# Kernel tuning notes

Measured on AMD Instinct MI355X. Metric: run time of the kernel, lower is better.

The kernel has to match this reference:

```python
import jax, jax.numpy as jnp
import numpy as np

NH = 16   # num_heads
HD = 128  # head_dim
HS = 2048 # hidden_size
LI, LT = 2048, 512
MLP = 4 * HS


def _ln(x, s, b):
    m = jnp.mean(x, axis=-1, keepdims=True)
    v = jnp.var(x, axis=-1, keepdims=True)
    return (x - m) * jax.lax.rsqrt(v + 1e-6) * s + b


def _rms(x, s):
    return x * jax.lax.rsqrt(jnp.mean(x * x, axis=-1, keepdims=True) + 1e-6) * s


def _mod6(vec, w, b):
    a = (jax.nn.silu(vec) @ w + b)[:, None, :]
    return jnp.split(a, 6, axis=-1)  # shift1,scale1,gate1,shift2,scale2,gate2


def _rope(x, pe):
    B, H, L, D = x.shape
    xr = x.reshape(B, H, L, D // 2, 1, 2)
    return (pe[..., 0] * xr[..., 0] + pe[..., 1] * xr[..., 1]).reshape(B, H, L, D)


def _attention(q, k, v, pe):
    q = _rope(q, pe)
    k = _rope(k, pe)
    scores = jnp.einsum('bhqd,bhkd->bhqk', q, k) * (q.shape[-1] ** -0.5)
    p = jax.nn.softmax(scores, axis=-1)
    o = jnp.einsum('bhqk,bhkd->bhqd', p, v)
    B, H, L, D = o.shape
    return o.transpose(0, 2, 1, 3).reshape(B, L, H * D)


def _prenorm_qkv(x, shift, scale, ln_s, ln_b, qkv_w, qkv_b, qn, kn):
    xm = (1.0 + scale) * _ln(x, ln_s, ln_b) + shift
    y = xm @ qkv_w + qkv_b
    B, L, _ = y.shape
    y = y.reshape(B, L, 3, NH, HD).transpose(2, 0, 3, 1, 4)  # K B H L D
    q, k, v = y[0], y[1], y[2]
    return _rms(q, qn), _rms(k, kn), v


def _forward(img, txt, vec, pe,
             img_mod_w, img_mod_b, img_norm1_s, img_norm1_b, img_qkv_w, img_qkv_b,
             img_qn_s, img_kn_s, img_proj_w, img_proj_b, img_norm2_s, img_norm2_b,
             img_mlp_w1, img_mlp_b1, img_mlp_w2, img_mlp_b2,
             txt_mod_w, txt_mod_b, txt_norm1_s, txt_norm1_b, txt_qkv_w, txt_qkv_b,
             txt_qn_s, txt_kn_s, txt_proj_w, txt_proj_b, txt_norm2_s, txt_norm2_b,
             txt_mlp_w1, txt_mlp_b1, txt_mlp_w2, txt_mlp_b2):
    i_sh1, i_sc1, i_g1, i_sh2, i_sc2, i_g2 = _mod6(vec, img_mod_w, img_mod_b)
    t_sh1, t_sc1, t_g1, t_sh2, t_sc2, t_g2 = _mod6(vec, txt_mod_w, txt_mod_b)

    iq, ik, iv = _prenorm_qkv(img, i_sh1, i_sc1, img_norm1_s, img_norm1_b,
                              img_qkv_w, img_qkv_b, img_qn_s, img_kn_s)
    tq, tk, tv = _prenorm_qkv(txt, t_sh1, t_sc1, txt_norm1_s, txt_norm1_b,
                              txt_qkv_w, txt_qkv_b, txt_qn_s, txt_kn_s)

    q = jnp.concatenate((tq, iq), axis=2)
    k = jnp.concatenate((tk, ik), axis=2)
    v = jnp.concatenate((tv, iv), axis=2)
    attn = _attention(q, k, v, pe)  # [B, LT+LI, HS]
    Lt = txt.shape[1]
    txt_attn, img_attn = attn[:, :Lt], attn[:, Lt:]

    img = img + i_g1 * (img_attn @ img_proj_w + img_proj_b)
    img_h = (1.0 + i_sc2) * _ln(img, img_norm2_s, img_norm2_b) + i_sh2
    img = img + i_g2 * (jax.nn.gelu(img_h @ img_mlp_w1 + img_mlp_b1) @ img_mlp_w2 + img_mlp_b2)

    txt = txt + t_g1 * (txt_attn @ txt_proj_w + txt_proj_b)
    txt_h = (1.0 + t_sc2) * _ln(txt, txt_norm2_s, txt_norm2_b) + t_sh2
    txt = txt + t_g2 * (jax.nn.gelu(txt_h @ txt_mlp_w1 + txt_mlp_b1) @ txt_mlp_w2 + txt_mlp_b2)
    return img, txt


def setup_inputs() -> dict:
    key = jax.random.key(0)
    ki = iter(jax.random.split(key, 48))
    def n(shape, s=0.02):
        return jax.random.normal(next(ki), shape, jnp.float32) * s
    d = {
        'img': jax.random.normal(next(ki), (1, LI, HS), jnp.float32),
        'txt': jax.random.normal(next(ki), (1, LT, HS), jnp.float32),
        'vec': jax.random.normal(next(ki), (1, HS), jnp.float32),
        'pe': jax.random.normal(next(ki), (1, 1, LT + LI, HD // 2, 2, 2), jnp.float32),
    }
    for p in ('img', 'txt'):
        d[p + '_mod_w'] = n((HS, 6 * HS)); d[p + '_mod_b'] = jnp.zeros((6 * HS,), jnp.float32)
        d[p + '_norm1_s'] = jnp.ones((HS,), jnp.float32); d[p + '_norm1_b'] = jnp.zeros((HS,), jnp.float32)
        d[p + '_qkv_w'] = n((HS, 3 * HS)); d[p + '_qkv_b'] = jnp.zeros((3 * HS,), jnp.float32)
        d[p + '_qn_s'] = jnp.ones((HD,), jnp.float32); d[p + '_kn_s'] = jnp.ones((HD,), jnp.float32)
        d[p + '_proj_w'] = n((HS, HS)); d[p + '_proj_b'] = jnp.zeros((HS,), jnp.float32)
        d[p + '_norm2_s'] = jnp.ones((HS,), jnp.float32); d[p + '_norm2_b'] = jnp.zeros((HS,), jnp.float32)
        d[p + '_mlp_w1'] = n((HS, MLP)); d[p + '_mlp_b1'] = jnp.zeros((MLP,), jnp.float32)
        d[p + '_mlp_w2'] = n((MLP, HS)); d[p + '_mlp_b2'] = jnp.zeros((HS,), jnp.float32)
    return d


def reference(img, txt, vec, pe,
              img_mod_w, img_mod_b, img_norm1_s, img_norm1_b, img_qkv_w, img_qkv_b,
              img_qn_s, img_kn_s, img_proj_w, img_proj_b, img_norm2_s, img_norm2_b,
              img_mlp_w1, img_mlp_b1, img_mlp_w2, img_mlp_b2,
              txt_mod_w, txt_mod_b, txt_norm1_s, txt_norm1_b, txt_qkv_w, txt_qkv_b,
              txt_qn_s, txt_kn_s, txt_proj_w, txt_proj_b, txt_norm2_s, txt_norm2_b,
              txt_mlp_w1, txt_mlp_b1, txt_mlp_w2, txt_mlp_b2):
    return _forward(img, txt, vec, pe,
                    img_mod_w, img_mod_b, img_norm1_s, img_norm1_b, img_qkv_w, img_qkv_b,
                    img_qn_s, img_kn_s, img_proj_w, img_proj_b, img_norm2_s, img_norm2_b,
                    img_mlp_w1, img_mlp_b1, img_mlp_w2, img_mlp_b2,
                    txt_mod_w, txt_mod_b, txt_norm1_s, txt_norm1_b, txt_qkv_w, txt_qkv_b,
                    txt_qn_s, txt_kn_s, txt_proj_w, txt_proj_b, txt_norm2_s, txt_norm2_b,
                    txt_mlp_w1, txt_mlp_b1, txt_mlp_w2, txt_mlp_b2)
```

## Files before the change

### kernel.cpp

```cpp
#include <hip/hip_runtime.h>
#include <hip/hip_bf16.h>
#include <math.h>

typedef __bf16 bf16;
typedef __bf16 bf16x2 __attribute__((ext_vector_type(2)));
typedef __bf16 bf16x8 __attribute__((ext_vector_type(8)));
typedef float f32x4 __attribute__((ext_vector_type(4)));

#define HS 2048
#define NH 16
#define HD 128
#define LT 512
#define LI 2048
#define LQ 2560
#define MLP_D 8192
#define SPLIT 4
#define KVS (LQ / SPLIT)
#define KVBLK 32
#define NTILES (KVS / KVBLK)

__device__ __forceinline__ f32x4 mfma16(bf16x8 a, bf16x8 b, f32x4 c) {
  return __builtin_amdgcn_mfma_f32_16x16x32_bf16(a, b, c, 0, 0, 0);
}

__device__ __forceinline__ void gl_lds16(const bf16* g, bf16* l) {
  __builtin_amdgcn_global_load_lds((const __attribute__((address_space(1))) void*)g,
                                   (__attribute__((address_space(3))) void*)l, 16, 0, 0);
}

__global__ void k_silu(const float* __restrict__ v, float* __restrict__ s) {
  int i = blockIdx.x * 256 + threadIdx.x;
  float x = v[i];
  s[i] = x / (1.f + expf(-x));
}

__global__ __launch_bounds__(256) void k_mod_partial(
    const float* __restrict__ s, const float* __restrict__ w_txt,
    const float* __restrict__ w_img, float* __restrict__ part) {
  int strm = blockIdx.x / 48;
  int n = (blockIdx.x % 48) * 256 + threadIdx.x;
  const float* w = strm ? w_img : w_txt;
  int k0 = blockIdx.y * 256;
  __shared__ float sl[256];
  sl[threadIdx.x] = s[k0 + threadIdx.x];
  __syncthreads();
  float acc = 0.f;
  for (int k = 0; k < 256; k++)
    acc += sl[k] * w[(size_t)(k0 + k) * 12288 + n];
  part[((size_t)blockIdx.y * 2 + strm) * 12288 + n] = acc;
}

__global__ __launch_bounds__(256) void k_mod_reduce(
    const float* __restrict__ part, const float* __restrict__ b_txt,
    const float* __restrict__ b_img, float* __restrict__ mod) {
  int strm = blockIdx.x / 48;
  int n = (blockIdx.x % 48) * 256 + threadIdx.x;
  float acc = strm ? b_img[n] : b_txt[n];
  for (int kc = 0; kc < 8; kc++)
    acc += part[((size_t)kc * 2 + strm) * 12288 + n];
  mod[(size_t)strm * 12288 + n] = acc;
}

__global__ __launch_bounds__(256) void k_transpose_cvt(
    const float* __restrict__ src, bf16* __restrict__ dst, int R, int C) {
  __shared__ float t[32][33];
  int tx = threadIdx.x & 31, ty = threadIdx.x >> 5;
  int c0 = blockIdx.x * 32, r0 = blockIdx.y * 32;
  for (int i = 0; i < 32; i += 8)
    t[ty + i][tx] = src[(size_t)(r0 + ty + i) * C + c0 + tx];
  __syncthreads();
  for (int i = 0; i < 32; i += 8)
    dst[(size_t)(c0 + ty + i) * R + r0 + tx] = (bf16)t[tx][ty + i];
}

__global__ __launch_bounds__(256) void k_ln_mod(
    const float* __restrict__ x0, const float* __restrict__ x1,
    const float* __restrict__ ls0, const float* __restrict__ lb0,
    const float* __restrict__ ls1, const float* __restrict__ lb1,
    const float* __restrict__ mod0, const float* __restrict__ mod1,
    int shidx, int scidx, bf16* __restrict__ out) {
  int r = blockIdx.x;
  int strm = r >= LT;
  const float* x = strm ? (x1 + (size_t)(r - LT) * HS) : (x0 + (size_t)r * HS);
  const float* ls = strm ? ls1 : ls0;
  const float* lb = strm ? lb1 : lb0;
  const float* md = strm ? mod1 : mod0;
  const float* sh = md + (size_t)shidx * HS;
  const float* sc = md + (size_t)scidx * HS;
  int t = threadIdx.x;
  float4 a = ((const float4*)x)[t * 2];
  float4 b = ((const float4*)x)[t * 2 + 1];
  float xv[8] = {a.x, a.y, a.z, a.w, b.x, b.y, b.z, b.w};
  float sum = 0.f, sq = 0.f;
#pragma unroll
  for (int j = 0; j < 8; j++) { sum += xv[j]; sq += xv[j] * xv[j]; }
#pragma unroll
  for (int m = 32; m; m >>= 1) { sum += __shfl_xor(sum, m); sq += __shfl_xor(sq, m); }
  __shared__ float red[8];
  int lane = t & 63, wid = t >> 6;
  if (!lane) { red[wid] = sum; red[wid + 4] = sq; }
  __syncthreads();
  float ts = red[0] + red[1] + red[2] + red[3];
  float tq = red[4] + red[5] + red[6] + red[7];
  float mean = ts * (1.f / HS);
  float var = tq * (1.f / HS) - mean * mean;
  float inv = rsqrtf(var + 1e-6f);
  int c0 = t * 8;
  bf16x8 ov;
#pragma unroll
  for (int j = 0; j < 8; j++) {
    int c = c0 + j;
    float v = ((xv[j] - mean) * inv * ls[c] + lb[c]) * (1.f + sc[c]) + sh[c];
    ov[j] = (bf16)v;
  }
  *(bf16x8*)(out + (size_t)r * HS + c0) = ov;
}

template <int MODE>
__global__ __launch_bounds__(256) void k_gemm(
    const bf16* __restrict__ A, int K, int N, int Ksz,
    const bf16* __restrict__ BT0, const bf16* __restrict__ BT1,
    const float* __restrict__ bias0, const float* __restrict__ bias1,
    void* __restrict__ out0, void* __restrict__ out1) {
  __shared__ bf16 As[128 * 32];
  __shared__ bf16 Bs[128 * 32];
  int tid = threadIdx.x;
  int bn = blockIdx.x, bm = blockIdx.y;
  int strm = (bm * 128) >= LT;
  int lm = bm * 128 - strm * LT;
  const bf16* BT = strm ? BT1 : BT0;
  int lane = tid & 63, wid = tid >> 6;
  int wr = wid >> 1, wc = wid & 1;
  int sr = tid >> 2, sc8 = (tid & 3) * 8;
  const bf16* Ag = A + (size_t)(bm * 128 + sr) * K + sc8;
  const bf16* Bg = BT + (size_t)(bn * 128 + sr) * K + sc8;
  bf16* As_dst = As + wid * 512;
  bf16* Bs_dst = Bs + wid * 512;
  int kbeg = MODE == 4 ? blockIdx.z * Ksz : 0;
  f32x4 acc[4][4] = {};
  for (int k0 = kbeg; k0 < kbeg + Ksz; k0 += 32) {
    __syncthreads();
    gl_lds16(Ag + k0, As_dst);
    gl_lds16(Ag + (size_t)64 * K + k0, As_dst + 2048);
    gl_lds16(Bg + k0, Bs_dst);
    gl_lds16(Bg + (size_t)64 * K + k0, Bs_dst + 2048);
    __syncthreads();
    bf16x8 af[4], bfr[4];
    int r16 = lane & 15, kc8 = (lane >> 4) * 8;
#pragma unroll
    for (int m = 0; m < 4; m++) af[m] = *(const bf16x8*)&As[(wr * 64 + m * 16 + r16) * 32 + kc8];
#pragma unroll
    for (int n = 0; n < 4; n++) bfr[n] = *(const bf16x8*)&Bs[(wc * 64 + n * 16 + r16) * 32 + kc8];
#pragma unroll
    for (int m = 0; m < 4; m++)
#pragma unroll
      for (int n = 0; n < 4; n++)
        acc[m][n] = mfma16(af[m], bfr[n], acc[m][n]);
  }
  int col = lane & 15, rb = (lane >> 4) * 4;
  const float* bias = strm ? bias1 : bias0;
  float* part = MODE == 4 ? (float*)out0 + (size_t)blockIdx.z * LQ * N : nullptr;
#pragma unroll
  for (int m = 0; m < 4; m++) {
#pragma unroll
    for (int n = 0; n < 4; n++) {
      int gn = bn * 128 + wc * 64 + n * 16 + col;
      float bv = MODE == 4 ? 0.f : bias[gn];
#pragma unroll
      for (int r = 0; r < 4; r++) {
        int lr = wr * 64 + m * 16 + rb + r;
        float v = acc[m][n][r] + bv;
        if (MODE == 0) {
          ((bf16*)(strm ? out1 : out0))[(size_t)(lm + lr) * N + gn] = (bf16)v;
        } else if (MODE == 2) {
          float g = 0.5f * v * (1.f + tanhf(0.7978845608028654f * (v + 0.044715f * v * v * v)));
          ((bf16*)(strm ? out1 : out0))[(size_t)(lm + lr) * N + gn] = (bf16)g;
        } else {
          part[(size_t)(bm * 128 + lr) * N + gn] = v;
        }
      }
    }
  }
}

template <int S>
__global__ __launch_bounds__(256) void k_skcomb(
    const float* __restrict__ part, int N,
    const float* __restrict__ bias0, const float* __restrict__ bias1,
    const float* __restrict__ gate0, const float* __restrict__ gate1,
    const float* __restrict__ res0, const float* __restrict__ res1,
    float* __restrict__ out0, float* __restrict__ out1) {
  int gid = blockIdx.x * 256 + threadIdx.x;
  int nv = N >> 2;
  int row = gid / nv, cv = gid - row * nv;
  int strm = row >= LT;
  int lrow = row - strm * LT;
  const float* bias = strm ? bias1 : bias0;
  const float* gate = strm ? gate1 : gate0;
  const float* res = strm ? res1 : res0;
  float* out = strm ? out1 : out0;
  int c = cv * 4;
  float4 acc = *(const float4*)(bias + c);
#pragma unroll
  for (int s = 0; s < S; s++) {
    float4 p = *(const float4*)(part + ((size_t)s * LQ + row) * N + c);
    acc.x += p.x; acc.y += p.y; acc.z += p.z; acc.w += p.w;
  }
  float4 g = *(const float4*)(gate + c);
  float4 r = *(const float4*)(res + (size_t)lrow * N + c);
  float4 o = {r.x + g.x * acc.x, r.y + g.y * acc.y, r.z + g.z * acc.z, r.w + g.w * acc.w};
  *(float4*)(out + (size_t)lrow * N + c) = o;
}

__global__ __launch_bounds__(256) void k_qkv_post(
    const bf16* __restrict__ y, const float* __restrict__ pe,
    const float* __restrict__ qn0, const float* __restrict__ kn0,
    const float* __restrict__ qn1, const float* __restrict__ kn1,
    bf16* __restrict__ qh, bf16* __restrict__ kh) {
  int wv = (int)((blockIdx.x * 256 + threadIdx.x) >> 6);
  int lane = threadIdx.x & 63;
  int head = wv / LQ, l = wv - head * LQ;
  const bf16* yr = y + (size_t)l * (3 * HS) + head * HD;
  float q0 = (float)yr[2 * lane], q1 = (float)yr[2 * lane + 1];
  float k0 = (float)yr[HS + 2 * lane], k1 = (float)yr[HS + 2 * lane + 1];
  float sqs = q0 * q0 + q1 * q1, sks = k0 * k0 + k1 * k1;
#pragma unroll
  for (int m = 1; m < 64; m <<= 1) { sqs += __shfl_xor(sqs, m); sks += __shfl_xor(sks, m); }
  float rq = rsqrtf(sqs * (1.f / HD) + 1e-6f);
  float rk = rsqrtf(sks * (1.f / HD) + 1e-6f);
  int strm = l >= LT;
  const float* qn = strm ? qn1 : qn0;
  const float* kn = strm ? kn1 : kn0;
  float e0 = q0 * rq * qn[2 * lane], e1 = q1 * rq * qn[2 * lane + 1];
  float f0 = k0 * rk * kn[2 * lane], f1 = k1 * rk * kn[2 * lane + 1];
  float4 p = *(const float4*)(pe + ((size_t)l * 64 + lane) * 4);
  const float scl = 0.08838834764831845f;
  size_t qi = ((size_t)head * LQ + l) * HD + 2 * lane;
  bf16x2 qv = {(bf16)((p.x * e0 + p.y * e1) * scl), (bf16)((p.z * e0 + p.w * e1) * scl)};
  bf16x2 kv = {(bf16)(p.x * f0 + p.y * f1), (bf16)(p.z * f0 + p.w * f1)};
  *(bf16x2*)(qh + qi) = qv;
  *(bf16x2*)(kh + qi) = kv;
}

__global__ __launch_bounds__(256) void k_vtrans(const bf16* __restrict__ y,
                                                bf16* __restrict__ vT) {
  __shared__ bf16 t[32][34];
  int head = blockIdx.y >> 2, dt = blockIdx.y & 3;
  int tx = threadIdx.x & 31, ty = threadIdx.x >> 5;
  int l0 = blockIdx.x * 32, d0 = dt * 32;
  for (int i = 0; i < 32; i += 8)
    t[ty + i][tx] = y[(size_t)(l0 + ty + i) * (3 * HS) + 2 * HS + head * HD + d0 + tx];
  __syncthreads();
  for (int i = 0; i < 32; i += 8)
    vT[(size_t)(head * HD + d0 + ty + i) * LQ + l0 + tx] = t[tx][ty + i];
}

__global__ __launch_bounds__(256, 5) void k_attn(
    const bf16* __restrict__ Q, const bf16* __restrict__ Kh,
    const bf16* __restrict__ VT, bf16* __restrict__ Op, float* __restrict__ ml) {
  __shared__ bf16 Ks[KVBLK * 128];
  __shared__ bf16 Vs[128 * KVBLK];
  __shared__ bf16 P[4][16 * 34];
  int tid = threadIdx.x, lane = tid & 63, w = tid >> 6;
  int b = blockIdx.x;
  int qb = b % 40;
  int split = (b / 40) % SPLIT;
  int head = b / (40 * SPLIT);
  int qr = qb * 64 + w * 16;
  int r16 = lane & 15, g = lane >> 4;
  const bf16* qp = Q + ((size_t)head * LQ + qr + r16) * HD + g * 8;
  bf16x8 qf[4];
#pragma unroll
  for (int c = 0; c < 4; c++) qf[c] = *(const bf16x8*)(qp + c * 32);
  f32x4 O[8] = {};
  float mr[4], lr[4];
#pragma unroll
  for (int i = 0; i < 4; i++) { mr[i] = -1e30f; lr[i] = 0.f; }
  bf16* pl = &P[w][0];
  const bf16* kbase = Kh + ((size_t)head * LQ + split * KVS) * HD;
  const bf16* vbase = VT + (size_t)head * HD * LQ + split * KVS;
  int krow0 = w * 8 + (lane >> 4);
  int kslot = lane & 15;
  int vrow0 = w * 32 + (lane >> 2);
  int vcol = (lane & 3) * 8;
  for (int t = 0; t < NTILES; t++) {
    int kv0 = t * KVBLK;
#pragma unroll
    for (int i = 0; i < 2; i++) {
      int krow = krow0 + i * 4;
      gl_lds16(kbase + (size_t)(kv0 + krow) * HD + ((kslot ^ (krow & 7)) << 3),
               Ks + (w * 8 + i * 4) * 128);
      int vrow = vrow0 + i * 16;
      gl_lds16(vbase + (size_t)vrow * LQ + kv0 + vcol,
               Vs + (w * 32 + i * 16) * KVBLK);
    }
    __syncthreads();
    f32x4 S0 = {}, S1 = {};
    int sw = (r16 & 7);
#pragma unroll
    for (int c = 0; c < 4; c++) {
      int slot = ((4 * c + g) ^ sw) << 3;
      bf16x8 ka = *(const bf16x8*)&Ks[r16 * 128 + slot];
      bf16x8 kb = *(const bf16x8*)&Ks[(16 + r16) * 128 + slot];
      S0 = mfma16(qf[c], ka, S0);
      S1 = mfma16(qf[c], kb, S1);
    }
    float alpha[4];
#pragma unroll
    for (int i = 0; i < 4; i++) {
      float mx = fmaxf(S0[i], S1[i]);
#pragma unroll
      for (int m = 8; m; m >>= 1) mx = fmaxf(mx, __shfl_xor(mx, m));
      float mn = fmaxf(mr[i], mx);
      float p0 = __expf(S0[i] - mn), p1 = __expf(S1[i] - mn);
      float rs = p0 + p1;
#pragma unroll
      for (int m = 8; m; m >>= 1) rs += __shfl_xor(rs, m);
      alpha[i] = __expf(mr[i] - mn);
      lr[i] = lr[i] * alpha[i] + rs;
      mr[i] = mn;
      pl[(4 * g + i) * 34 + r16] = (bf16)p0;
      pl[(4 * g + i) * 34 + 16 + r16] = (bf16)p1;
    }
    bf16x8 pf = *(const bf16x8*)&pl[r16 * 34 + g * 8];
#pragma unroll
    for (int n = 0; n < 8; n++) {
      f32x4 o = O[n];
#pragma unroll
      for (int i = 0; i < 4; i++) o[i] *= alpha[i];
      bf16x8 vf = *(const bf16x8*)&Vs[(n * 16 + r16) * KVBLK + g * 8];
      O[n] = mfma16(pf, vf, o);
    }
    __syncthreads();
  }
  const int NL = NH * LQ;
  bf16* op = Op + (size_t)split * NL * HD;
#pragma unroll
  for (int n = 0; n < 8; n++)
#pragma unroll
    for (int i = 0; i < 4; i++)
      op[((size_t)head * LQ + qr + 4 * g + i) * HD + n * 16 + r16] = (bf16)O[n][i];
  if (r16 == 0) {
#pragma unroll
    for (int i = 0; i < 4; i++) {
      int idx = head * LQ + qr + 4 * g + i;
      ml[(size_t)(split * 2 + 0) * NL + idx] = mr[i];
      ml[(size_t)(split * 2 + 1) * NL + idx] = lr[i];
    }
  }
}

__global__ __launch_bounds__(256) void k_attn_combine(
    const bf16* __restrict__ Op, const float* __restrict__ ml, bf16* __restrict__ out) {
  int lane = threadIdx.x & 63, w = threadIdx.x >> 6;
  int row = blockIdx.x * 4 + w;
  int head = row / LQ, l = row - head * LQ;
  const int NL = NH * LQ;
  float ms[SPLIT], ls[SPLIT], m = -1e30f;
#pragma unroll
  for (int s = 0; s < SPLIT; s++) {
    ms[s] = ml[(size_t)(s * 2) * NL + row];
    ls[s] = ml[(size_t)(s * 2 + 1) * NL + row];
    m = fmaxf(m, ms[s]);
  }
  float wsum = 0.f, wgt[SPLIT];
#pragma unroll
  for (int s = 0; s < SPLIT; s++) { wgt[s] = __expf(ms[s] - m); wsum += wgt[s] * ls[s]; }
  float inv = 1.f / wsum;
  size_t oi = (size_t)row * HD + 2 * lane;
  float a0 = 0.f, a1 = 0.f;
#pragma unroll
  for (int s = 0; s < SPLIT; s++) {
    bf16x2 v = *(const bf16x2*)(Op + (size_t)s * NL * HD + oi);
    a0 += wgt[s] * (float)v[0];
    a1 += wgt[s] * (float)v[1];
  }
  bf16x2 ov = {(bf16)(a0 * inv), (bf16)(a1 * inv)};
  *(bf16x2*)(out + (size_t)l * HS + head * HD + 2 * lane) = ov;
}

extern "C" void kernel_launch(void* const* d_in, const int* in_sizes, int n_in,
                              void* d_out, int out_size, void* d_ws, size_t ws_size,
                              hipStream_t stream) {
  const float* img = (const float*)d_in[0];
  const float* txt = (const float*)d_in[1];
  const float* vec = (const float*)d_in[2];
  const float* pe = (const float*)d_in[3];
#define PARAM(i) ((const float*)d_in[i])

  char* ws = (char*)d_ws;
  size_t off = 0;
  auto alloc = [&](size_t b) { void* p = ws + off; off += (b + 255) & ~(size_t)255; return p; };
  float* silu_s = (float*)alloc((size_t)HS * 4);
  float* mpart = (float*)alloc((size_t)8 * 2 * 12288 * 4);
  float* mod = (float*)alloc((size_t)2 * 6 * HS * 4);
  bf16* qkvT0 = (bf16*)alloc((size_t)3 * HS * HS * 2);
  bf16* qkvT1 = (bf16*)alloc((size_t)3 * HS * HS * 2);
  bf16* projT0 = (bf16*)alloc((size_t)HS * HS * 2);
  bf16* projT1 = (bf16*)alloc((size_t)HS * HS * 2);
  bf16* mlp1T0 = (bf16*)alloc((size_t)MLP_D * HS * 2);
  bf16* mlp1T1 = (bf16*)alloc((size_t)MLP_D * HS * 2);
  bf16* mlp2T0 = (bf16*)alloc((size_t)HS * MLP_D * 2);
  bf16* mlp2T1 = (bf16*)alloc((size_t)HS * MLP_D * 2);
  bf16* xm = (bf16*)alloc((size_t)LQ * HS * 2);
  bf16* y = (bf16*)alloc((size_t)LQ * 3 * HS * 2);
  bf16* qh = (bf16*)alloc((size_t)NH * LQ * HD * 2);
  bf16* kh = (bf16*)alloc((size_t)NH * LQ * HD * 2);
  bf16* vT = (bf16*)alloc((size_t)NH * HD * LQ * 2);
  bf16* attnb = (bf16*)alloc((size_t)LQ * HS * 2);
  float* x2 = (float*)alloc((size_t)LQ * HS * 4);
  bf16* xm2 = (bf16*)alloc((size_t)LQ * HS * 2);
  bf16* h = (bf16*)alloc((size_t)LQ * MLP_D * 2);
  float* ml = (float*)alloc((size_t)2 * SPLIT * NH * LQ * 4);
  bf16* Op = h;
  float* skpart = (float*)xm;
  (void)ws_size; (void)in_sizes; (void)n_in; (void)out_size;

  const float* t_mod = mod;
  const float* i_mod = mod + 6 * HS;

  k_silu<<<HS / 256, 256, 0, stream>>>(vec, silu_s);
  k_mod_partial<<<dim3(96, 8), 256, 0, stream>>>(silu_s, PARAM(20), PARAM(4), mpart);
  k_mod_reduce<<<96, 256, 0, stream>>>(mpart, PARAM(21), PARAM(5), mod);

  k_transpose_cvt<<<dim3(3 * HS / 32, HS / 32), 256, 0, stream>>>(PARAM(24), qkvT0, HS, 3 * HS);
  k_transpose_cvt<<<dim3(3 * HS / 32, HS / 32), 256, 0, stream>>>(PARAM(8), qkvT1, HS, 3 * HS);
  k_transpose_cvt<<<dim3(HS / 32, HS / 32), 256, 0, stream>>>(PARAM(28), projT0, HS, HS);
  k_transpose_cvt<<<dim3(HS / 32, HS / 32), 256, 0, stream>>>(PARAM(12), projT1, HS, HS);
  k_transpose_cvt<<<dim3(MLP_D / 32, HS / 32), 256, 0, stream>>>(PARAM(32), mlp1T0, HS, MLP_D);
  k_transpose_cvt<<<dim3(MLP_D / 32, HS / 32), 256, 0, stream>>>(PARAM(16), mlp1T1, HS, MLP_D);
  k_transpose_cvt<<<dim3(HS / 32, MLP_D / 32), 256, 0, stream>>>(PARAM(34), mlp2T0, MLP_D, HS);
  k_transpose_cvt<<<dim3(HS / 32, MLP_D / 32), 256, 0, stream>>>(PARAM(18), mlp2T1, MLP_D, HS);

  k_ln_mod<<<LQ, 256, 0, stream>>>(txt, img, PARAM(22), PARAM(23), PARAM(6), PARAM(7),
                                   t_mod, i_mod, 0, 1, xm);

  k_gemm<0><<<dim3(3 * HS / 128, LQ / 128), 256, 0, stream>>>(
      xm, HS, 3 * HS, HS, qkvT0, qkvT1, PARAM(25), PARAM(9), y, y + (size_t)LT * 3 * HS);

  k_qkv_post<<<NH * LQ / 4, 256, 0, stream>>>(y, pe, PARAM(26), PARAM(27), PARAM(10), PARAM(11),
                                              qh, kh);
  k_vtrans<<<dim3(LQ / 32, NH * 4), 256, 0, stream>>>(y, vT);

  k_attn<<<NH * SPLIT * 40, 256, 0, stream>>>(qh, kh, vT, Op, ml);
  k_attn_combine<<<NH * LQ / 4, 256, 0, stream>>>(Op, ml, attnb);

  k_gemm<4><<<dim3(HS / 128, LQ / 128, 2), 256, 0, stream>>>(
      attnb, HS, HS, HS / 2, projT0, projT1, nullptr, nullptr, skpart, nullptr);
  k_skcomb<2><<<LQ * HS / 4 / 256, 256, 0, stream>>>(
      skpart, HS, PARAM(29), PARAM(13), t_mod + 2 * HS, i_mod + 2 * HS, txt, img,
      x2, x2 + (size_t)LT * HS);

  k_ln_mod<<<LQ, 256, 0, stream>>>(x2, x2 + (size_t)LT * HS, PARAM(30), PARAM(31), PARAM(14),
                                   PARAM(15), t_mod, i_mod, 3, 4, xm2);

  k_gemm<2><<<dim3(MLP_D / 128, LQ / 128), 256, 0, stream>>>(
      xm2, HS, MLP_D, HS, mlp1T0, mlp1T1, PARAM(33), PARAM(17), h, h + (size_t)LT * MLP_D);

  float* out_img = (float*)d_out;
  float* out_txt = (float*)d_out + (size_t)LI * HS;
  k_gemm<4><<<dim3(HS / 128, LQ / 128, 4), 256, 0, stream>>>(
      h, MLP_D, HS, MLP_D / 4, mlp2T0, mlp2T1, nullptr, nullptr, skpart, nullptr);
  k_skcomb<4><<<LQ * HS / 4 / 256, 256, 0, stream>>>(
      skpart, HS, PARAM(35), PARAM(19), t_mod + 5 * HS, i_mod + 5 * HS, x2,
      x2 + (size_t)LT * HS, out_txt, out_img);
}
```

Baseline: 874.1 us.

## Double-buffer attention K/V tiles, swizzle V LDS, widen weight transpose tiles

The attention kernel now keeps two LDS buffers for K and V. It prefetches the next tile while computing the current one, which removes the trailing barrier per iteration. V staging and reads use an XOR swizzle to cut LDS bank conflicts. The transpose-convert kernel moves to 64x64 tiles with 16-byte vectorized bf16 stores. Occupancy hint for attention drops from 5 to 4 blocks per CU to fit the larger LDS footprint.

```diff
diff --git a/kernel.cpp b/kernel.cpp
--- a/kernel.cpp
+++ b/kernel.cpp
@@ -63,14 +63,21 @@
 
 __global__ __launch_bounds__(256) void k_transpose_cvt(
     const float* __restrict__ src, bf16* __restrict__ dst, int R, int C) {
-  __shared__ float t[32][33];
-  int tx = threadIdx.x & 31, ty = threadIdx.x >> 5;
-  int c0 = blockIdx.x * 32, r0 = blockIdx.y * 32;
-  for (int i = 0; i < 32; i += 8)
+  __shared__ float t[64][65];
+  int tx = threadIdx.x & 63, ty = threadIdx.x >> 6;
+  int c0 = blockIdx.x * 64, r0 = blockIdx.y * 64;
+  for (int i = 0; i < 64; i += 4)
     t[ty + i][tx] = src[(size_t)(r0 + ty + i) * C + c0 + tx];
   __syncthreads();
-  for (int i = 0; i < 32; i += 8)
-    dst[(size_t)(c0 + ty + i) * R + r0 + tx] = (bf16)t[tx][ty + i];
+#pragma unroll
+  for (int j = 0; j < 2; j++) {
+    int c = (threadIdx.x >> 3) + j * 32;
+    int gg = (threadIdx.x & 7) * 8;
+    bf16x8 ov;
+#pragma unroll
+    for (int k = 0; k < 8; k++) ov[k] = (bf16)t[gg + k][c];
+    *(bf16x8*)(dst + (size_t)(c0 + c) * R + r0 + gg) = ov;
+  }
 }
 
 __global__ __launch_bounds__(256) void k_ln_mod(
@@ -255,11 +262,11 @@
     vT[(size_t)(head * HD + d0 + ty + i) * LQ + l0 + tx] = t[tx][ty + i];
 }
 
-__global__ __launch_bounds__(256, 5) void k_attn(
+__global__ __launch_bounds__(256, 4) void k_attn(
     const bf16* __restrict__ Q, const bf16* __restrict__ Kh,
     const bf16* __restrict__ VT, bf16* __restrict__ Op, float* __restrict__ ml) {
-  __shared__ bf16 Ks[KVBLK * 128];
-  __shared__ bf16 Vs[128 * KVBLK];
+  __shared__ bf16 Ks[2][KVBLK * 128];
+  __shared__ bf16 Vs[2][128 * KVBLK];
   __shared__ bf16 P[4][16 * 34];
   int tid = threadIdx.x, lane = tid & 63, w = tid >> 6;
   int b = blockIdx.x;
@@ -282,26 +289,33 @@
   int krow0 = w * 8 + (lane >> 4);
   int kslot = lane & 15;
   int vrow0 = w * 32 + (lane >> 2);
-  int vcol = (lane & 3) * 8;
-  for (int t = 0; t < NTILES; t++) {
+  int vslot = lane & 3;
+  auto stage = [&](int buf, int t) {
     int kv0 = t * KVBLK;
 #pragma unroll
     for (int i = 0; i < 2; i++) {
       int krow = krow0 + i * 4;
       gl_lds16(kbase + (size_t)(kv0 + krow) * HD + ((kslot ^ (krow & 7)) << 3),
-               Ks + (w * 8 + i * 4) * 128);
+               &Ks[buf][(w * 8 + i * 4) * 128]);
       int vrow = vrow0 + i * 16;
-      gl_lds16(vbase + (size_t)vrow * LQ + kv0 + vcol,
-               Vs + (w * 32 + i * 16) * KVBLK);
-    }
+      gl_lds16(vbase + (size_t)vrow * LQ + kv0 + ((vslot ^ (vrow & 3)) << 3),
+               &Vs[buf][(w * 32 + i * 16) * KVBLK]);
+    }
+  };
+  stage(0, 0);
+  int cur = 0;
+  for (int t = 0; t < NTILES; t++) {
     __syncthreads();
+    if (t + 1 < NTILES) stage(cur ^ 1, t + 1);
+    const bf16* ks = &Ks[cur][0];
+    const bf16* vs = &Vs[cur][0];
     f32x4 S0 = {}, S1 = {};
     int sw = (r16 & 7);
 #pragma unroll
     for (int c = 0; c < 4; c++) {
       int slot = ((4 * c + g) ^ sw) << 3;
-      bf16x8 ka = *(const bf16x8*)&Ks[r16 * 128 + slot];
-      bf16x8 kb = *(const bf16x8*)&Ks[(16 + r16) * 128 + slot];
+      bf16x8 ka = *(const bf16x8*)&ks[r16 * 128 + slot];
+      bf16x8 kb = *(const bf16x8*)&ks[(16 + r16) * 128 + slot];
       S0 = mfma16(qf[c], ka, S0);
       S1 = mfma16(qf[c], kb, S1);
     }
@@ -323,15 +337,16 @@
       pl[(4 * g + i) * 34 + 16 + r16] = (bf16)p1;
     }
     bf16x8 pf = *(const bf16x8*)&pl[r16 * 34 + g * 8];
+    int vsl = (g ^ (r16 & 3)) * 8;
 #pragma unroll
     for (int n = 0; n < 8; n++) {
       f32x4 o = O[n];
 #pragma unroll
       for (int i = 0; i < 4; i++) o[i] *= alpha[i];
-      bf16x8 vf = *(const bf16x8*)&Vs[(n * 16 + r16) * KVBLK + g * 8];
+      bf16x8 vf = *(const bf16x8*)&vs[(n * 16 + r16) * KVBLK + vsl];
       O[n] = mfma16(pf, vf, o);
     }
-    __syncthreads();
+    cur ^= 1;
   }
   const int NL = NH * LQ;
   bf16* op = Op + (size_t)split * NL * HD;
@@ -423,14 +438,14 @@
   k_mod_partial<<<dim3(96, 8), 256, 0, stream>>>(silu_s, PARAM(20), PARAM(4), mpart);
   k_mod_reduce<<<96, 256, 0, stream>>>(mpart, PARAM(21), PARAM(5), mod);
 
-  k_transpose_cvt<<<dim3(3 * HS / 32, HS / 32), 256, 0, stream>>>(PARAM(24), qkvT0, HS, 3 * HS);
-  k_transpose_cvt<<<dim3(3 * HS / 32, HS / 32), 256, 0, stream>>>(PARAM(8), qkvT1, HS, 3 * HS);
-  k_transpose_cvt<<<dim3(HS / 32, HS / 32), 256, 0, stream>>>(PARAM(28), projT0, HS, HS);
-  k_transpose_cvt<<<dim3(HS / 32, HS / 32), 256, 0, stream>>>(PARAM(12), projT1, HS, HS);
-  k_transpose_cvt<<<dim3(MLP_D / 32, HS / 32), 256, 0, stream>>>(PARAM(32), mlp1T0, HS, MLP_D);
-  k_transpose_cvt<<<dim3(MLP_D / 32, HS / 32), 256, 0, stream>>>(PARAM(16), mlp1T1, HS, MLP_D);
-  k_transpose_cvt<<<dim3(HS / 32, MLP_D / 32), 256, 0, stream>>>(PARAM(34), mlp2T0, MLP_D, HS);
-  k_transpose_cvt<<<dim3(HS / 32, MLP_D / 32), 256, 0, stream>>>(PARAM(18), mlp2T1, MLP_D, HS);
+  k_transpose_cvt<<<dim3(3 * HS / 64, HS / 64), 256, 0, stream>>>(PARAM(24), qkvT0, HS, 3 * HS);
+  k_transpose_cvt<<<dim3(3 * HS / 64, HS / 64), 256, 0, stream>>>(PARAM(8), qkvT1, HS, 3 * HS);
+  k_transpose_cvt<<<dim3(HS / 64, HS / 64), 256, 0, stream>>>(PARAM(28), projT0, HS, HS);
+  k_transpose_cvt<<<dim3(HS / 64, HS / 64), 256, 0, stream>>>(PARAM(12), projT1, HS, HS);
+  k_transpose_cvt<<<dim3(MLP_D / 64, HS / 64), 256, 0, stream>>>(PARAM(32), mlp1T0, HS, MLP_D);
+  k_transpose_cvt<<<dim3(MLP_D / 64, HS / 64), 256, 0, stream>>>(PARAM(16), mlp1T1, HS, MLP_D);
+  k_transpose_cvt<<<dim3(HS / 64, MLP_D / 64), 256, 0, stream>>>(PARAM(34), mlp2T0, MLP_D, HS);
+  k_transpose_cvt<<<dim3(HS / 64, MLP_D / 64), 256, 0, stream>>>(PARAM(18), mlp2T1, MLP_D, HS);
 
   k_ln_mod<<<LQ, 256, 0, stream>>>(txt, img, PARAM(22), PARAM(23), PARAM(6), PARAM(7),
                                    t_mod, i_mod, 0, 1, xm);
```

Measured after the change: 860.4 us. No clear change (-1.6%).
